# Performance work log

Measured on AMD Instinct MI355X. Metric: run time of the kernel, lower is better.

Reference implementation:

```python
import jax, jax.numpy as jnp
jax.config.update("jax_enable_x64", True)
import numpy as np

LEAF = 0.3          # leaf_voxel_size
FACTOR = 2.0        # scale_up_factor
LEVELS = 3          # voxel_level_num
DIM = 8             # feature_dim
BUF = 5000000       # hash_buffer_size
NFEAT = 4194304     # entries per level feature table
PRIMES = jnp.array([73856093, 19349669, 83492791], dtype=jnp.int64)
STEPS = jnp.array([[0.,0.,0.],[0.,0.,1.],[0.,1.,0.],[0.,1.,1.],
                   [1.,0.,0.],[1.,0.,1.],[1.,1.,0.],[1.,1.,1.]], dtype=jnp.float32)

def setup_inputs() -> dict:
    key = jax.random.key(0)
    k1, k2, k3 = jax.random.split(key, 3)
    query_points = jax.random.normal(k1, (1000000, 3), dtype=jnp.float32) * 25.0
    features = 0.01 * jax.random.normal(k2, (LEVELS, NFEAT, DIM), dtype=jnp.float32)
    index_table = jax.random.randint(k3, (LEVELS, BUF), 0, NFEAT, dtype=jnp.int64)
    return {"query_points": query_points, "features": features, "index_table": index_table}

def _level_features(points, feats, idx_table, res):
    # points: [N,3], feats: [F,D], idx_table: [BUF] int64
    base = jnp.floor(points / res)                       # [N,3]
    corners = base[:, None, :] + STEPS[None]             # [N,8,3]
    keys = (corners.astype(jnp.int64) * PRIMES).sum(-1) % BUF  # [N,8]
    idx = idx_table[keys]                                # [N,8]
    mask = idx.min(axis=1) > -1                          # point valid iff all 8 corners mapped
    gathered = feats[jnp.maximum(idx, 0)]                # [N,8,D]
    d = points / res - base                              # fractional coords in cell, [N,3]
    # trilinear weights, corner order matches STEPS (same as torch interpolat)
    w = (STEPS[None] * d[:, None, :] + (1.0 - STEPS[None]) * (1.0 - d[:, None, :])).prod(-1)  # [N,8]
    lvl = (gathered * w[..., None]).sum(1)               # [N,D]
    return jnp.where(mask[:, None], lvl, 0.0)

def reference(query_points, features, index_table):
    out = jnp.zeros((query_points.shape[0], DIM), dtype=jnp.float32)
    for i in range(LEVELS):
        res = LEAF * FACTOR ** i
        out = out + _level_features(query_points, features[i], index_table[i], res)
    return out
```

## Files before the change

kernel.cpp:

```cpp
#include <hip/hip_runtime.h>


constexpr int       BUF   = 5000000;
constexpr long long NFEAT = 4194304;
constexpr int       DIM   = 8;
constexpr long long P0 = 73856093, P1 = 19349669, P2 = 83492791;

typedef float vf4 __attribute__((ext_vector_type(4)));

#define GLD0(dst, voff, base)                                  \
    asm volatile("global_load_dwordx4 %0, %1, %2"              \
                 : "=v"(dst) : "v"(voff), "s"(base))
#define GLD16(dst, voff, base)                                 \
    asm volatile("global_load_dwordx4 %0, %1, %2 offset:16"    \
                 : "=v"(dst) : "v"(voff), "s"(base))

template <bool ADD>
__global__ __launch_bounds__(256, 4) void nvh_level_kernel(
    const float* __restrict__ qp,
    const float* __restrict__ fb,
    const int* __restrict__ tab,
    float* __restrict__ out, int n, float res)
{
    int i = blockIdx.x * blockDim.x + threadIdx.x;
    if (i >= n) return;

    const float px = qp[3 * i + 0];
    const float py = qp[3 * i + 1];
    const float pz = qp[3 * i + 2];

    const float fx = px / res, fy = py / res, fz = pz / res;
    const float bx = floorf(fx), by = floorf(fy), bz = floorf(fz);
    const float dx = fx - bx, dy = fy - by, dz = fz - bz;

    const long long ix = (long long)bx;
    const long long iy = (long long)by;
    const long long iz = (long long)bz;

    long long h0 = (ix * P0 + iy * P1 + iz * P2) % (long long)BUF;
    if (h0 < 0) h0 += BUF;
    const int k0 = (int)h0;

    int idxv[8];
#pragma unroll
    for (int c = 0; c < 8; ++c) {
        const long long offc = (((c >> 2) & 1) * P0 + ((c >> 1) & 1) * P1 +
                                (c & 1) * P2) % (long long)BUF;
        int k = k0 + (int)offc;
        if (k >= BUF) k -= BUF;
        idxv[c] = tab[k];
    }
    __builtin_amdgcn_sched_barrier(0);

    bool valid = true;
    unsigned voff[8];
#pragma unroll
    for (int c = 0; c < 8; ++c) {
        valid = valid && (idxv[c] > -1);
        const int id = idxv[c] > 0 ? idxv[c] : 0;
        voff[c] = (unsigned)id * 32u;
    }

    vf4 f[16];
#pragma unroll
    for (int c = 0; c < 8; ++c) {
        GLD0 (f[2 * c + 0], voff[c], fb);
        GLD16(f[2 * c + 1], voff[c], fb);
    }

    vf4 prev0, prev1;
    if (ADD) {
        const vf4* op = (const vf4*)(out + (size_t)i * DIM);
        prev0 = op[0];
        prev1 = op[1];
    }

    const float wx1 = dx, wx0 = 1.0f - dx;
    const float wy1 = dy, wy0 = 1.0f - dy;
    const float wz1 = dz, wz0 = 1.0f - dz;
    const float vmask = valid ? 1.0f : 0.0f;

    asm volatile("s_waitcnt vmcnt(0)" ::: "memory");
    __builtin_amdgcn_sched_barrier(0);

    vf4 lacc0 = (vf4)0.0f;
    vf4 lacc1 = (vf4)0.0f;
#pragma unroll
    for (int c = 0; c < 8; ++c) {
        const float wc = (((c >> 2) & 1) ? wx1 : wx0) *
                         (((c >> 1) & 1) ? wy1 : wy0) *
                         (((c     ) & 1) ? wz1 : wz0);
        lacc0 += wc * f[2 * c + 0];
        lacc1 += wc * f[2 * c + 1];
    }

    vf4 r0 = vmask * lacc0;
    vf4 r1 = vmask * lacc1;
    if (ADD) { r0 += prev0; r1 += prev1; }

    vf4* op = (vf4*)(out + (size_t)i * DIM);
    op[0] = r0;
    op[1] = r1;
}

extern "C" void kernel_launch(void* const* d_in, const int* in_sizes, int n_in,
                              void* d_out, int out_size, void* d_ws, size_t ws_size,
                              hipStream_t stream) {
    const float* qp      = (const float*)d_in[0];
    const float* feats   = (const float*)d_in[1];
    const int*   idx_tab = (const int*)d_in[2];
    float*       out     = (float*)d_out;

    const int n = in_sizes[0] / 3;
    const int block = 256;
    const int grid = (n + block - 1) / block;

    hipLaunchKernelGGL((nvh_level_kernel<false>), dim3(grid), dim3(block), 0,
                       stream, qp, feats, idx_tab, out, n, 0.3f);
    hipLaunchKernelGGL((nvh_level_kernel<true>), dim3(grid), dim3(block), 0,
                       stream, qp, feats + (size_t)1 * NFEAT * DIM,
                       idx_tab + (size_t)1 * BUF, out, n, 0.6f);
    hipLaunchKernelGGL((nvh_level_kernel<true>), dim3(grid), dim3(block), 0,
                       stream, qp, feats + (size_t)2 * NFEAT * DIM,
                       idx_tab + (size_t)2 * BUF, out, n, 1.2f);
}
```

Baseline: 1.258 ms.

## Sort query points by Morton order of coarse cells before level gathers

Adds a counting sort of query points by a Morton key of their coarsest-level cell, built from a histogram, a multi-block prefix scan and an atomic scatter. The three level kernels then run on the permuted points and a scratch output, and a final kernel un-permutes the results. The aim is for neighbouring threads to hit nearby cells, so table and feature gathers share cache lines and are more likely to hit in cache. In exchange it adds about eight extra launches, a 2M-bin histogram pass and extra permutation traffic, and it falls back to the old path when the workspace is too small.

```diff
diff --git a/kernel.cpp b/kernel.cpp
--- a/kernel.cpp
+++ b/kernel.cpp
@@ -5,6 +5,7 @@
 constexpr long long NFEAT = 4194304;
 constexpr int       DIM   = 8;
 constexpr long long P0 = 73856093, P1 = 19349669, P2 = 83492791;
+constexpr int       NBINS = 1 << 21;
 
 typedef float vf4 __attribute__((ext_vector_type(4)));
 
@@ -17,17 +18,18 @@
 
 template <bool ADD>
 __global__ __launch_bounds__(256, 4) void nvh_level_kernel(
-    const float* __restrict__ qp,
+    const float* __restrict__ in,
     const float* __restrict__ fb,
     const int* __restrict__ tab,
-    float* __restrict__ out, int n, float res)
-{
-    int i = blockIdx.x * blockDim.x + threadIdx.x;
-    if (i >= n) return;
-
-    const float px = qp[3 * i + 0];
-    const float py = qp[3 * i + 1];
-    const float pz = qp[3 * i + 2];
+    float* __restrict__ outp,
+    int n, float res)
+{
+    int i = blockIdx.x * blockDim.x + threadIdx.x;
+    if (i >= n) return;
+
+    const float px = in[3 * i + 0];
+    const float py = in[3 * i + 1];
+    const float pz = in[3 * i + 2];
 
     const float fx = px / res, fy = py / res, fz = pz / res;
     const float bx = floorf(fx), by = floorf(fy), bz = floorf(fz);
@@ -70,7 +72,7 @@
 
     vf4 prev0, prev1;
     if (ADD) {
-        const vf4* op = (const vf4*)(out + (size_t)i * DIM);
+        const vf4* op = (const vf4*)(outp + (size_t)i * DIM);
         prev0 = op[0];
         prev1 = op[1];
     }
@@ -98,9 +100,135 @@
     vf4 r1 = vmask * lacc1;
     if (ADD) { r0 += prev0; r1 += prev1; }
 
-    vf4* op = (vf4*)(out + (size_t)i * DIM);
+    vf4* op = (vf4*)(outp + (size_t)i * DIM);
     op[0] = r0;
     op[1] = r1;
+}
+
+__device__ __forceinline__ unsigned spread3(unsigned v) {
+    v = (v | (v << 16)) & 0x030000FFu;
+    v = (v | (v << 8))  & 0x0300F00Fu;
+    v = (v | (v << 4))  & 0x030C30C3u;
+    v = (v | (v << 2))  & 0x09249249u;
+    return v;
+}
+
+__global__ __launch_bounds__(256) void zero_hist(unsigned* __restrict__ h) {
+    int i = blockIdx.x * blockDim.x + threadIdx.x;
+    for (int k = i; k < NBINS; k += gridDim.x * blockDim.x) h[k] = 0u;
+}
+
+__global__ __launch_bounds__(256) void keys_hist(
+    const float* __restrict__ qp, unsigned* __restrict__ keys,
+    unsigned* __restrict__ hist, int n)
+{
+    int i = blockIdx.x * blockDim.x + threadIdx.x;
+    if (i >= n) return;
+    const float inv = 1.0f / 1.2f;
+    int cx = (int)floorf(qp[3 * i + 0] * inv);
+    int cy = (int)floorf(qp[3 * i + 1] * inv);
+    int cz = (int)floorf(qp[3 * i + 2] * inv);
+    cx = cx < -64 ? -64 : (cx > 63 ? 63 : cx);
+    cy = cy < -64 ? -64 : (cy > 63 ? 63 : cy);
+    cz = cz < -64 ? -64 : (cz > 63 ? 63 : cz);
+    const unsigned key = (spread3((unsigned)(cx + 64)) << 2) |
+                         (spread3((unsigned)(cy + 64)) << 1) |
+                          spread3((unsigned)(cz + 64));
+    keys[i] = key;
+    atomicAdd(&hist[key], 1u);
+}
+
+__global__ __launch_bounds__(256) void scan_blocks(
+    unsigned* __restrict__ data, unsigned* __restrict__ bsum)
+{
+    __shared__ unsigned s[256];
+    const int t = threadIdx.x;
+    const int base = blockIdx.x * 1024 + t * 4;
+    unsigned v0 = data[base + 0], v1 = data[base + 1];
+    unsigned v2 = data[base + 2], v3 = data[base + 3];
+    const unsigned tsum = v0 + v1 + v2 + v3;
+    s[t] = tsum;
+    __syncthreads();
+    for (int off = 1; off < 256; off <<= 1) {
+        unsigned x = (t >= off) ? s[t - off] : 0u;
+        __syncthreads();
+        s[t] += x;
+        __syncthreads();
+    }
+    const unsigned excl = s[t] - tsum;
+    if (t == 255) bsum[blockIdx.x] = s[255];
+    data[base + 0] = excl;
+    data[base + 1] = excl + v0;
+    data[base + 2] = excl + v0 + v1;
+    data[base + 3] = excl + v0 + v1 + v2;
+}
+
+__global__ __launch_bounds__(256) void scan_top(unsigned* __restrict__ bsum) {
+    __shared__ unsigned s[256];
+    const int t = threadIdx.x;
+    unsigned v[8];
+    unsigned tsum = 0;
+#pragma unroll
+    for (int j = 0; j < 8; ++j) { v[j] = bsum[t * 8 + j]; tsum += v[j]; }
+    s[t] = tsum;
+    __syncthreads();
+    for (int off = 1; off < 256; off <<= 1) {
+        unsigned x = (t >= off) ? s[t - off] : 0u;
+        __syncthreads();
+        s[t] += x;
+        __syncthreads();
+    }
+    unsigned run = s[t] - tsum;
+#pragma unroll
+    for (int j = 0; j < 8; ++j) { const unsigned nv = run; run += v[j]; bsum[t * 8 + j] = nv; }
+}
+
+__global__ __launch_bounds__(256) void scan_add(
+    unsigned* __restrict__ data, const unsigned* __restrict__ bsum)
+{
+    const int base = blockIdx.x * 1024 + threadIdx.x * 4;
+    const unsigned add = bsum[blockIdx.x];
+    data[base + 0] += add;
+    data[base + 1] += add;
+    data[base + 2] += add;
+    data[base + 3] += add;
+}
+
+__global__ __launch_bounds__(256) void scatter_perm(
+    const unsigned* __restrict__ keys, unsigned* __restrict__ hist,
+    unsigned* __restrict__ perm, unsigned* __restrict__ invp, int n)
+{
+    int i = blockIdx.x * blockDim.x + threadIdx.x;
+    if (i >= n) return;
+    const unsigned r = atomicAdd(&hist[keys[i]], 1u);
+    perm[r] = (unsigned)i;
+    invp[i] = r;
+}
+
+__global__ __launch_bounds__(256) void gather_points(
+    const float* __restrict__ qp, const unsigned* __restrict__ perm,
+    float* __restrict__ qps, int n)
+{
+    int i = blockIdx.x * blockDim.x + threadIdx.x;
+    if (i >= n) return;
+    const unsigned j = perm[i];
+    qps[3 * i + 0] = qp[3 * j + 0];
+    qps[3 * i + 1] = qp[3 * j + 1];
+    qps[3 * i + 2] = qp[3 * j + 2];
+}
+
+__global__ __launch_bounds__(256) void unpermute_out(
+    const float* __restrict__ out_s, const unsigned* __restrict__ invp,
+    float* __restrict__ out, int n)
+{
+    int i = blockIdx.x * blockDim.x + threadIdx.x;
+    if (i >= n) return;
+    const unsigned r = invp[i];
+    const vf4* a = (const vf4*)(out_s + (size_t)r * DIM);
+    const vf4 x = a[0], y = a[1];
+    vf4* o = (vf4*)(out + (size_t)i * DIM);
+    o[0] = x;
+    o[1] = y;
 }
 
 extern "C" void kernel_launch(void* const* d_in, const int* in_sizes, int n_in,
@@ -115,12 +243,66 @@
     const int block = 256;
     const int grid = (n + block - 1) / block;
 
-    hipLaunchKernelGGL((nvh_level_kernel<false>), dim3(grid), dim3(block), 0,
-                       stream, qp, feats, idx_tab, out, n, 0.3f);
-    hipLaunchKernelGGL((nvh_level_kernel<true>), dim3(grid), dim3(block), 0,
-                       stream, qp, feats + (size_t)1 * NFEAT * DIM,
-                       idx_tab + (size_t)1 * BUF, out, n, 0.6f);
-    hipLaunchKernelGGL((nvh_level_kernel<true>), dim3(grid), dim3(block), 0,
-                       stream, qp, feats + (size_t)2 * NFEAT * DIM,
-                       idx_tab + (size_t)2 * BUF, out, n, 1.2f);
-}
+    auto al = [](size_t x) { return (x + 255) & ~(size_t)255; };
+    const size_t o_hist = 0;
+    const size_t o_bsum = al(o_hist + (size_t)NBINS * 4);
+    const size_t o_keys = al(o_bsum + 2048 * 4);
+    const size_t o_perm = al(o_keys + (size_t)n * 4);
+    const size_t o_invp = al(o_perm + (size_t)n * 4);
+    const size_t o_qps  = al(o_invp + (size_t)n * 4);
+    const size_t o_outs = al(o_qps  + (size_t)n * 12);
+    const size_t need   = o_outs + (size_t)n * 32;
+
+    const bool use_sort = (d_ws != nullptr) && (ws_size >= need);
+
+    const float* in_pts = qp;
+    float*       out_l  = out;
+
+    if (use_sort) {
+        char* ws = (char*)d_ws;
+        unsigned* hist = (unsigned*)(ws + o_hist);
+        unsigned* bsum = (unsigned*)(ws + o_bsum);
+        unsigned* keys = (unsigned*)(ws + o_keys);
+        unsigned* perm = (unsigned*)(ws + o_perm);
+        unsigned* invp = (unsigned*)(ws + o_invp);
+        float*    qps  = (float*)   (ws + o_qps);
+        float*    outs = (float*)   (ws + o_outs);
+
+        hipLaunchKernelGGL(zero_hist, dim3(2048), dim3(block), 0, stream, hist);
+        hipLaunchKernelGGL(keys_hist, dim3(grid), dim3(block), 0, stream,
+                           qp, keys, hist, n);
+        hipLaunchKernelGGL(scan_blocks, dim3(NBINS / 1024), dim3(block), 0,
+                           stream, hist, bsum);
+        hipLaunchKernelGGL(scan_top, dim3(1), dim3(block), 0, stream, bsum);
+        hipLaunchKernelGGL(scan_add, dim3(NBINS / 1024), dim3(block), 0,
+                           stream, hist, bsum);
+        hipLaunchKernelGGL(scatter_perm, dim3(grid), dim3(block), 0, stream,
+                           keys, hist, perm, invp, n);
+        hipLaunchKernelGGL(gather_points, dim3(grid), dim3(block), 0, stream,
+                           qp, perm, qps, n);
+
+        in_pts = qps;
+        out_l  = outs;
+
+        hipLaunchKernelGGL((nvh_level_kernel<false>), dim3(grid), dim3(block),
+                           0, stream, in_pts, feats, idx_tab, out_l, n, 0.3f);
+        hipLaunchKernelGGL((nvh_level_kernel<true>), dim3(grid), dim3(block),
+                           0, stream, in_pts, feats + (size_t)1 * NFEAT * DIM,
+                           idx_tab + (size_t)1 * BUF, out_l, n, 0.6f);
+        hipLaunchKernelGGL((nvh_level_kernel<true>), dim3(grid), dim3(block),
+                           0, stream, in_pts, feats + (size_t)2 * NFEAT * DIM,
+                           idx_tab + (size_t)2 * BUF, out_l, n, 1.2f);
+
+        hipLaunchKernelGGL(unpermute_out, dim3(grid), dim3(block), 0, stream,
+                           outs, invp, out, n);
+    } else {
+        hipLaunchKernelGGL((nvh_level_kernel<false>), dim3(grid), dim3(block),
+                           0, stream, qp, feats, idx_tab, out, n, 0.3f);
+        hipLaunchKernelGGL((nvh_level_kernel<true>), dim3(grid), dim3(block),
+                           0, stream, qp, feats + (size_t)1 * NFEAT * DIM,
+                           idx_tab + (size_t)1 * BUF, out, n, 0.6f);
+        hipLaunchKernelGGL((nvh_level_kernel<true>), dim3(grid), dim3(block),
+                           0, stream, qp, feats + (size_t)2 * NFEAT * DIM,
+                           idx_tab + (size_t)2 * BUF, out, n, 1.2f);
+    }
+}
```

After: 1.099 ms. 12.6% less time.
